# Kernel optimization log

Hardware: AMD Instinct MI355X
Metric: run time of the kernel (lower is better)

Reference implementation:

```python
import jax, jax.numpy as jnp
import numpy as np

N_NODES = 50000
N_EDGES = 800000
D_IN = 256
D_HID = 256
D_OUT = 8


def _glorot(key, shape):
    fan_in = shape[-1]
    bound = 1.0 / np.sqrt(fan_in)
    return jax.random.uniform(key, shape, minval=-bound, maxval=bound, dtype=jnp.float32)


def setup_inputs() -> dict:
    key = jax.random.key(0)
    ks = jax.random.split(key, 12)
    x = jax.random.normal(ks[0], (N_NODES, D_IN), dtype=jnp.float32)
    edge_index = jax.random.randint(ks[1], (2, N_EDGES), 0, N_NODES, dtype=jnp.int64)
    return {
        "x": x,
        "edge_index": edge_index,
        # SAGEConv1: lin_l (neighbor path, has bias), lin_r (root path, no bias)
        "W1l": _glorot(ks[2], (D_HID, D_IN)),
        "b1": jnp.zeros((D_HID,), jnp.float32),
        "W1r": _glorot(ks[3], (D_HID, D_IN)),
        # SAGEConv2
        "W2l": _glorot(ks[4], (D_HID, D_HID)),
        "b2": jnp.zeros((D_HID,), jnp.float32),
        "W2r": _glorot(ks[5], (D_HID, D_HID)),
        # MLP decoder
        "Wm1": _glorot(ks[6], (D_HID, D_HID)),
        "bm1": _glorot(ks[7], (D_HID,)),
        "Wm2": _glorot(ks[8], (D_OUT, D_HID)),
        "bm2": _glorot(ks[9], (D_OUT,)),
    }


def _sage_conv(x, edge_index, Wl, b, Wr):
    # PyG SAGEConv with mean aggregation:
    # out = lin_l(mean_{j in N(i)} x_j) + lin_r(x_i)
    src, dst = edge_index[0], edge_index[1]
    msg = x[src]  # [E, d] gather
    agg = jax.ops.segment_sum(msg, dst, num_segments=x.shape[0])  # [N, d]
    cnt = jax.ops.segment_sum(jnp.ones((edge_index.shape[1],), x.dtype), dst,
                              num_segments=x.shape[0])  # in-degree [N]
    mean = agg / jnp.maximum(cnt, 1.0)[:, None]
    return mean @ Wl.T + b + x @ Wr.T


def reference(x, edge_index, W1l, b1, W1r, W2l, b2, W2r, Wm1, bm1, Wm2, bm2):
    h = jax.nn.relu(_sage_conv(x, edge_index, W1l, b1, W1r))
    h = jax.nn.relu(_sage_conv(h, edge_index, W2l, b2, W2r))
    h = jax.nn.relu(h @ Wm1.T + bm1)
    logits = h @ Wm2.T + bm2
    return jax.nn.softmax(logits, axis=-1)
```

## Files before the change

kernel.cpp:

```cpp
#include <hip/hip_runtime.h>
#include <math.h>

#define N_NODES 50000
#define N_EDGES 800000
#define D 256

typedef unsigned short u16;
typedef __attribute__((ext_vector_type(8))) __bf16 bf16x8;
typedef __attribute__((ext_vector_type(4))) float f32x4;

__device__ __forceinline__ void split_hi_lo(float v, u16& h, u16& l) {
    unsigned u = __float_as_uint(v);
    unsigned hh = (u + 0x7fff + ((u >> 16) & 1)) >> 16;
    float hf = __uint_as_float(hh << 16);
    float res = v - hf;
    unsigned ul = __float_as_uint(res);
    unsigned ll = (ul + 0x7fff + ((ul >> 16) & 1)) >> 16;
    h = (u16)hh; l = (u16)ll;
}

__device__ __forceinline__ float bflo(unsigned u) { return __uint_as_float(u << 16); }
__device__ __forceinline__ float bfhi(unsigned u) { return __uint_as_float(u & 0xffff0000u); }

__device__ __forceinline__ void gl_lds16(const void* g, void* l) {
    __builtin_amdgcn_global_load_lds(
        (const __attribute__((address_space(1))) void*)g,
        (__attribute__((address_space(3))) void*)l, 16, 0, 0);
}

__global__ void zero_i32(int* __restrict__ p, int n) {
    int i = blockIdx.x * blockDim.x + threadIdx.x;
    if (i < n) p[i] = 0;
}

__global__ void count_deg(const int* __restrict__ ei, int* __restrict__ cnt) {
    int e = blockIdx.x * blockDim.x + threadIdx.x;
    if (e < N_EDGES) atomicAdd(&cnt[ei[N_EDGES + e]], 1);
}

__global__ void scan1(const int* __restrict__ cnt, int* __restrict__ partial,
                      int* __restrict__ bsum) {
    __shared__ int s[1024];
    int t = threadIdx.x, b = blockIdx.x;
    int gid = b * 1024 + t;
    int v = (gid < N_NODES) ? cnt[gid] : 0;
    s[t] = v;
    __syncthreads();
    for (int off = 1; off < 1024; off <<= 1) {
        int u = (t >= off) ? s[t - off] : 0;
        __syncthreads();
        s[t] += u;
        __syncthreads();
    }
    partial[gid] = s[t];
    if (t == 1023) bsum[b] = s[1023];
}

__global__ void scan2(const int* __restrict__ bsum, int* __restrict__ boff, int nb) {
    int t = threadIdx.x;
    int orig = (t < nb) ? bsum[t] : 0;
    int v = orig;
    #pragma unroll
    for (int off = 1; off < 64; off <<= 1) {
        int u = __shfl_up(v, off, 64);
        if (t >= off) v += u;
    }
    boff[t] = v - orig;
}

__global__ void scan3(const int* __restrict__ partial, const int* __restrict__ boff,
                      int* __restrict__ rowptr, int* __restrict__ cursor) {
    int i = blockIdx.x * blockDim.x + threadIdx.x;
    if (i <= N_NODES) {
        int val = 0;
        if (i > 0) val = partial[i - 1] + boff[(i - 1) >> 10];
        rowptr[i] = val;
        if (i < N_NODES) cursor[i] = val;
    }
}

__global__ void fill_edges(const int* __restrict__ ei, int* __restrict__ cursor,
                           int* __restrict__ esrc) {
    int e = blockIdx.x * blockDim.x + threadIdx.x;
    if (e < N_EDGES) {
        int p = atomicAdd(&cursor[ei[N_EDGES + e]], 1);
        esrc[p] = ei[e];
    }
}

__global__ void split_bf16(const float* __restrict__ in, u16* __restrict__ hi,
                           u16* __restrict__ lo, int n) {
    int i = blockIdx.x * blockDim.x + threadIdx.x;
    if (i < n) {
        u16 h, l; split_hi_lo(in[i], h, l);
        hi[i] = h; lo[i] = l;
    }
}

__global__ __launch_bounds__(256) void aggregate_bf16(const u16* __restrict__ in_hi,
        const int* __restrict__ rowptr, const int* __restrict__ esrc,
        u16* __restrict__ ohi, u16* __restrict__ olo) {
    int node = blockIdx.x * 4 + (threadIdx.x >> 6);
    if (node >= N_NODES) return;
    int lane = threadIdx.x & 63;
    int half = lane >> 5;
    int sub = lane & 31;
    int beg = rowptr[node], end = rowptr[node + 1];
    const u16* rowp = in_hi + sub * 8;

    float a0 = 0.f, a1 = 0.f, a2 = 0.f, a3 = 0.f;
    float a4 = 0.f, a5 = 0.f, a6 = 0.f, a7 = 0.f;

#define ACC8(v) \
    a0 += bflo(v.x); a1 += bfhi(v.x); a2 += bflo(v.y); a3 += bfhi(v.y); \
    a4 += bflo(v.z); a5 += bfhi(v.z); a6 += bflo(v.w); a7 += bfhi(v.w);

    int j = beg;
    for (; j + 8 <= end; j += 8) {
        int i0 = esrc[j + 0 + half];
        int i1 = esrc[j + 2 + half];
        int i2 = esrc[j + 4 + half];
        int i3 = esrc[j + 6 + half];
        uint4 r0 = *(const uint4*)(rowp + (size_t)i0 * D);
        uint4 r1 = *(const uint4*)(rowp + (size_t)i1 * D);
        uint4 r2 = *(const uint4*)(rowp + (size_t)i2 * D);
        uint4 r3 = *(const uint4*)(rowp + (size_t)i3 * D);
        ACC8(r0); ACC8(r1); ACC8(r2); ACC8(r3);
    }
    for (; j < end; j += 2) {
        int e = j + half;
        if (e < end) {
            uint4 r = *(const uint4*)(rowp + (size_t)esrc[e] * D);
            ACC8(r);
        }
    }
#undef ACC8

    a0 += __shfl_xor(a0, 32, 64); a1 += __shfl_xor(a1, 32, 64);
    a2 += __shfl_xor(a2, 32, 64); a3 += __shfl_xor(a3, 32, 64);
    a4 += __shfl_xor(a4, 32, 64); a5 += __shfl_xor(a5, 32, 64);
    a6 += __shfl_xor(a6, 32, 64); a7 += __shfl_xor(a7, 32, 64);

    if (lane < 32) {
        float inv = 1.f / (float)max(end - beg, 1);
        float m[8] = { a0 * inv, a1 * inv, a2 * inv, a3 * inv,
                       a4 * inv, a5 * inv, a6 * inv, a7 * inv };
        u16 h[8], l[8];
        #pragma unroll
        for (int k = 0; k < 8; ++k) split_hi_lo(m[k], h[k], l[k]);
        size_t o = (size_t)node * D + lane * 8;
        *(uint4*)(ohi + o) = make_uint4(h[0] | (h[1] << 16), h[2] | (h[3] << 16),
                                        h[4] | (h[5] << 16), h[6] | (h[7] << 16));
        *(uint4*)(olo + o) = make_uint4(l[0] | (l[1] << 16), l[2] | (l[3] << 16),
                                        l[4] | (l[5] << 16), l[6] | (l[7] << 16));
    }
}

__global__ __launch_bounds__(256, 2) void gemm_mfma(
        const u16* __restrict__ A1h, const u16* __restrict__ A1l,
        const u16* __restrict__ A2h, const u16* __restrict__ A2l,
        const u16* __restrict__ B1h, const u16* __restrict__ B1l,
        const u16* __restrict__ B2h, const u16* __restrict__ B2l,
        const float* __restrict__ bias, int K, int relu,
        float* __restrict__ Cf, u16* __restrict__ Chi, u16* __restrict__ Clo) {
    __shared__ u16 lds[4][128 * 32];
    const int t = threadIdx.x;
    const int lane = t & 63;
    const int w = t >> 6;
    const int wm = (w >> 1) * 64, wn = (w & 1) * 64;
    const int m0 = blockIdx.x * 128, n0 = blockIdx.y * 128;

    f32x4 acc[4][4] = {};

    const int tr = t >> 2;
    const int g = (t & 3) ^ ((t >> 3) & 3);
    const int lm = lane & 15;
    const int sw = (((lane >> 4) ^ ((lm >> 1) & 3))) * 8;

    for (int k0 = 0; k0 < K; k0 += 32) {
        const u16 *Ah, *Al, *Bh, *Bl; int ks;
        if (k0 < 256) { Ah = A1h; Al = A1l; Bh = B1h; Bl = B1l; ks = k0; }
        else          { Ah = A2h; Al = A2l; Bh = B2h; Bl = B2l; ks = k0 - 256; }

        __syncthreads();
        #pragma unroll
        for (int r = 0; r < 2; ++r) {
            int arow = m0 + r * 64 + tr; if (arow >= N_NODES) arow = N_NODES - 1;
            size_t aoff = (size_t)arow * D + ks + g * 8;
            size_t boff = (size_t)(n0 + r * 64 + tr) * D + ks + g * 8;
            int dst = r * 2048 + t * 8;
            gl_lds16(Ah + aoff, &lds[0][dst]);
            gl_lds16(Al + aoff, &lds[1][dst]);
            gl_lds16(Bh + boff, &lds[2][dst]);
            gl_lds16(Bl + boff, &lds[3][dst]);
        }
        __syncthreads();

        bf16x8 ah[4], al[4], bh[4], bl[4];
        #pragma unroll
        for (int i = 0; i < 4; ++i) {
            int offA = (wm + i * 16 + lm) * 32 + sw;
            ah[i] = *(const bf16x8*)&lds[0][offA];
            al[i] = *(const bf16x8*)&lds[1][offA];
            int offB = (wn + i * 16 + lm) * 32 + sw;
            bh[i] = *(const bf16x8*)&lds[2][offB];
            bl[i] = *(const bf16x8*)&lds[3][offB];
        }
        #pragma unroll
        for (int i = 0; i < 4; ++i) {
            #pragma unroll
            for (int j = 0; j < 4; ++j) {
                acc[i][j] = __builtin_amdgcn_mfma_f32_16x16x32_bf16(ah[i], bh[j], acc[i][j], 0, 0, 0);
                acc[i][j] = __builtin_amdgcn_mfma_f32_16x16x32_bf16(ah[i], bl[j], acc[i][j], 0, 0, 0);
                acc[i][j] = __builtin_amdgcn_mfma_f32_16x16x32_bf16(al[i], bh[j], acc[i][j], 0, 0, 0);
            }
        }
    }

    const int q = lane >> 4;
    #pragma unroll
    for (int j = 0; j < 4; ++j) {
        int col = n0 + wn + j * 16 + lm;
        float bb = bias[col];
        #pragma unroll
        for (int i = 0; i < 4; ++i) {
            int rowb = m0 + wm + i * 16 + q * 4;
            #pragma unroll
            for (int r = 0; r < 4; ++r) {
                int row = rowb + r;
                if (row < N_NODES) {
                    float v = acc[i][j][r] + bb;
                    if (relu) v = fmaxf(v, 0.f);
                    size_t o = (size_t)row * D + col;
                    if (Cf) Cf[o] = v;
                    if (Chi) {
                        u16 h, l; split_hi_lo(v, h, l);
                        Chi[o] = h; Clo[o] = l;
                    }
                }
            }
        }
    }
}

__global__ __launch_bounds__(256) void mlp2_softmax(const float* __restrict__ h,
        const float* __restrict__ W, const float* __restrict__ b,
        float* __restrict__ out) {
    int wid = threadIdx.x >> 6;
    int lane = threadIdx.x & 63;
    int n = blockIdx.x * 4 + wid;
    if (n >= N_NODES) return;

    float4 hv = ((const float4*)(h + (size_t)n * D))[lane];
    float acc[8];
    #pragma unroll
    for (int o = 0; o < 8; ++o) {
        float4 w = ((const float4*)(W + o * D))[lane];
        acc[o] = hv.x * w.x + hv.y * w.y + hv.z * w.z + hv.w * w.w;
    }
    #pragma unroll
    for (int o = 0; o < 8; ++o) {
        #pragma unroll
        for (int off = 32; off >= 1; off >>= 1)
            acc[o] += __shfl_xor(acc[o], off, 64);
    }
    if (lane == 0) {
        float v[8];
        float m = -1e30f;
        #pragma unroll
        for (int o = 0; o < 8; ++o) { v[o] = acc[o] + b[o]; m = fmaxf(m, v[o]); }
        float s = 0.f;
        #pragma unroll
        for (int o = 0; o < 8; ++o) { v[o] = expf(v[o] - m); s += v[o]; }
        float inv = 1.f / s;
        float4 o0 = make_float4(v[0] * inv, v[1] * inv, v[2] * inv, v[3] * inv);
        float4 o1 = make_float4(v[4] * inv, v[5] * inv, v[6] * inv, v[7] * inv);
        ((float4*)(out + (size_t)n * 8))[0] = o0;
        ((float4*)(out + (size_t)n * 8))[1] = o1;
    }
}

static inline size_t align_up(size_t x) { return (x + 255) & ~(size_t)255; }

extern "C" void kernel_launch(void* const* d_in, const int* in_sizes, int n_in,
                              void* d_out, int out_size, void* d_ws, size_t ws_size,
                              hipStream_t stream) {
    const float* x   = (const float*)d_in[0];
    const int*   ei  = (const int*)d_in[1];
    const float* W1l = (const float*)d_in[2];
    const float* b1  = (const float*)d_in[3];
    const float* W1r = (const float*)d_in[4];
    const float* W2l = (const float*)d_in[5];
    const float* b2  = (const float*)d_in[6];
    const float* W2r = (const float*)d_in[7];
    const float* Wm1 = (const float*)d_in[8];
    const float* bm1 = (const float*)d_in[9];
    const float* Wm2 = (const float*)d_in[10];
    const float* bm2 = (const float*)d_in[11];
    float* out = (float*)d_out;

    const size_t NF = (size_t)N_NODES * D;
    const size_t NW = (size_t)D * D;

    char* w = (char*)d_ws;
    u16* x_hi  = (u16*)w; w += align_up(NF * 2);
    u16* x_lo  = (u16*)w; w += align_up(NF * 2);
    u16* mn_hi = (u16*)w; w += align_up(NF * 2 * 2);
    u16* mn_lo = mn_hi + NF;
    u16* h1_hi = (u16*)w; w += align_up(NF * 2);
    u16* h1_lo = (u16*)w; w += align_up(NF * 2);
    u16* h2_hi = (u16*)w; w += align_up(NF * 2);
    u16* h2_lo = (u16*)w; w += align_up(NF * 2);
    u16* wbuf  = (u16*)w; w += align_up(NW * 2 * 10);
    u16* w1l_h = wbuf + 0 * NW; u16* w1l_l = wbuf + 1 * NW;
    u16* w1r_h = wbuf + 2 * NW; u16* w1r_l = wbuf + 3 * NW;
    u16* w2l_h = wbuf + 4 * NW; u16* w2l_l = wbuf + 5 * NW;
    u16* w2r_h = wbuf + 6 * NW; u16* w2r_l = wbuf + 7 * NW;
    u16* wm1_h = wbuf + 8 * NW; u16* wm1_l = wbuf + 9 * NW;
    int* cnt     = (int*)w; w += align_up((size_t)N_NODES * 4);
    int* rowptr  = (int*)w; w += align_up((size_t)(N_NODES + 1) * 4);
    int* cursor  = (int*)w; w += align_up((size_t)N_NODES * 4);
    int* partial = (int*)w; w += align_up((size_t)49 * 1024 * 4);
    int* bsum    = (int*)w; w += align_up((size_t)64 * 4);
    int* boff    = (int*)w; w += align_up((size_t)64 * 4);
    int* esrc    = (int*)w; w += align_up((size_t)N_EDGES * 4);
    float* h3 = (float*)mn_hi;

    zero_i32<<<(N_NODES + 255) / 256, 256, 0, stream>>>(cnt, N_NODES);
    count_deg<<<(N_EDGES + 255) / 256, 256, 0, stream>>>(ei, cnt);
    scan1<<<49, 1024, 0, stream>>>(cnt, partial, bsum);
    scan2<<<1, 64, 0, stream>>>(bsum, boff, 49);
    scan3<<<(N_NODES + 256) / 256, 256, 0, stream>>>(partial, boff, rowptr, cursor);
    fill_edges<<<(N_EDGES + 255) / 256, 256, 0, stream>>>(ei, cursor, esrc);

    split_bf16<<<(int)((NF + 255) / 256), 256, 0, stream>>>(x, x_hi, x_lo, (int)NF);
    split_bf16<<<(int)((NW + 255) / 256), 256, 0, stream>>>(W1l, w1l_h, w1l_l, (int)NW);
    split_bf16<<<(int)((NW + 255) / 256), 256, 0, stream>>>(W1r, w1r_h, w1r_l, (int)NW);
    split_bf16<<<(int)((NW + 255) / 256), 256, 0, stream>>>(W2l, w2l_h, w2l_l, (int)NW);
    split_bf16<<<(int)((NW + 255) / 256), 256, 0, stream>>>(W2r, w2r_h, w2r_l, (int)NW);
    split_bf16<<<(int)((NW + 255) / 256), 256, 0, stream>>>(Wm1, wm1_h, wm1_l, (int)NW);

    dim3 ggrid((N_NODES + 127) / 128, 2);
    int agrid = (N_NODES + 3) / 4;

    aggregate_bf16<<<agrid, 256, 0, stream>>>(x_hi, rowptr, esrc, mn_hi, mn_lo);
    gemm_mfma<<<ggrid, 256, 0, stream>>>(mn_hi, mn_lo, x_hi, x_lo,
                                         w1l_h, w1l_l, w1r_h, w1r_l,
                                         b1, 512, 1, nullptr, h1_hi, h1_lo);
    aggregate_bf16<<<agrid, 256, 0, stream>>>(h1_hi, rowptr, esrc, mn_hi, mn_lo);
    gemm_mfma<<<ggrid, 256, 0, stream>>>(mn_hi, mn_lo, h1_hi, h1_lo,
                                         w2l_h, w2l_l, w2r_h, w2r_l,
                                         b2, 512, 1, nullptr, h2_hi, h2_lo);
    gemm_mfma<<<ggrid, 256, 0, stream>>>(h2_hi, h2_lo, h2_hi, h2_lo,
                                         wm1_h, wm1_l, wm1_h, wm1_l,
                                         bm1, 256, 1, h3, nullptr, nullptr);
    mlp2_softmax<<<(N_NODES + 3) / 4, 256, 0, stream>>>(h3, Wm2, bm2, out);
}
```

Measured before the change: 562.6 us.

## Double-buffer LDS tiles in MFMA GEMM to overlap global loads with compute

The GEMM kernel now keeps two LDS tile buffers. It issues the global-to-LDS loads for the next K-slice before running the MFMAs on the current slice, and waits with vmcnt(0) plus a barrier only after the compute. This is meant to hide global-memory latency behind matrix math and to cut one barrier per iteration. In exchange, LDS use per block doubles, from 32KB to 64KB, which can limit occupancy.

Result: no change. 563.8 us (+0.2%).

```diff
diff --git a/kernel.cpp b/kernel.cpp
--- a/kernel.cpp
+++ b/kernel.cpp
@@ -156,6 +156,23 @@
     }
 }
 
+__device__ __forceinline__ void stage_tile(u16 (*ldsb)[128 * 32],
+        const u16* __restrict__ Ah, const u16* __restrict__ Al,
+        const u16* __restrict__ Bh, const u16* __restrict__ Bl,
+        int ks, int m0, int n0, int t, int tr, int g) {
+    #pragma unroll
+    for (int r = 0; r < 2; ++r) {
+        int arow = m0 + r * 64 + tr; if (arow >= N_NODES) arow = N_NODES - 1;
+        size_t aoff = (size_t)arow * D + ks + g * 8;
+        size_t boff = (size_t)(n0 + r * 64 + tr) * D + ks + g * 8;
+        int dst = r * 2048 + t * 8;
+        gl_lds16(Ah + aoff, &ldsb[0][dst]);
+        gl_lds16(Al + aoff, &ldsb[1][dst]);
+        gl_lds16(Bh + boff, &ldsb[2][dst]);
+        gl_lds16(Bl + boff, &ldsb[3][dst]);
+    }
+}
+
 __global__ __launch_bounds__(256, 2) void gemm_mfma(
         const u16* __restrict__ A1h, const u16* __restrict__ A1l,
         const u16* __restrict__ A2h, const u16* __restrict__ A2l,
@@ -163,7 +180,7 @@
         const u16* __restrict__ B2h, const u16* __restrict__ B2l,
         const float* __restrict__ bias, int K, int relu,
         float* __restrict__ Cf, u16* __restrict__ Chi, u16* __restrict__ Clo) {
-    __shared__ u16 lds[4][128 * 32];
+    __shared__ u16 lds[2][4][128 * 32];
     const int t = threadIdx.x;
     const int lane = t & 63;
     const int w = t >> 6;
@@ -177,34 +194,35 @@
     const int lm = lane & 15;
     const int sw = (((lane >> 4) ^ ((lm >> 1) & 3))) * 8;
 
+    {
+        const u16 *Ah, *Al, *Bh, *Bl;
+        Ah = A1h; Al = A1l; Bh = B1h; Bl = B1l;
+        stage_tile(lds[0], Ah, Al, Bh, Bl, 0, m0, n0, t, tr, g);
+    }
+    asm volatile("s_waitcnt vmcnt(0)" ::: "memory");
+    __builtin_amdgcn_s_barrier();
+
+    int cur = 0;
     for (int k0 = 0; k0 < K; k0 += 32) {
-        const u16 *Ah, *Al, *Bh, *Bl; int ks;
-        if (k0 < 256) { Ah = A1h; Al = A1l; Bh = B1h; Bl = B1l; ks = k0; }
-        else          { Ah = A2h; Al = A2l; Bh = B2h; Bl = B2l; ks = k0 - 256; }
-
-        __syncthreads();
-        #pragma unroll
-        for (int r = 0; r < 2; ++r) {
-            int arow = m0 + r * 64 + tr; if (arow >= N_NODES) arow = N_NODES - 1;
-            size_t aoff = (size_t)arow * D + ks + g * 8;
-            size_t boff = (size_t)(n0 + r * 64 + tr) * D + ks + g * 8;
-            int dst = r * 2048 + t * 8;
-            gl_lds16(Ah + aoff, &lds[0][dst]);
-            gl_lds16(Al + aoff, &lds[1][dst]);
-            gl_lds16(Bh + boff, &lds[2][dst]);
-            gl_lds16(Bl + boff, &lds[3][dst]);
-        }
-        __syncthreads();
+        const int nxt = cur ^ 1;
+        const bool has_next = (k0 + 32 < K);
+        if (has_next) {
+            int k1 = k0 + 32;
+            const u16 *Ah, *Al, *Bh, *Bl; int ks;
+            if (k1 < 256) { Ah = A1h; Al = A1l; Bh = B1h; Bl = B1l; ks = k1; }
+            else          { Ah = A2h; Al = A2l; Bh = B2h; Bl = B2l; ks = k1 - 256; }
+            stage_tile(lds[nxt], Ah, Al, Bh, Bl, ks, m0, n0, t, tr, g);
+        }
 
         bf16x8 ah[4], al[4], bh[4], bl[4];
         #pragma unroll
         for (int i = 0; i < 4; ++i) {
             int offA = (wm + i * 16 + lm) * 32 + sw;
-            ah[i] = *(const bf16x8*)&lds[0][offA];
-            al[i] = *(const bf16x8*)&lds[1][offA];
+            ah[i] = *(const bf16x8*)&lds[cur][0][offA];
+            al[i] = *(const bf16x8*)&lds[cur][1][offA];
             int offB = (wn + i * 16 + lm) * 32 + sw;
-            bh[i] = *(const bf16x8*)&lds[2][offB];
-            bl[i] = *(const bf16x8*)&lds[3][offB];
+            bh[i] = *(const bf16x8*)&lds[cur][2][offB];
+            bl[i] = *(const bf16x8*)&lds[cur][3][offB];
         }
         #pragma unroll
         for (int i = 0; i < 4; ++i) {
@@ -214,6 +232,12 @@
                 acc[i][j] = __builtin_amdgcn_mfma_f32_16x16x32_bf16(ah[i], bl[j], acc[i][j], 0, 0, 0);
                 acc[i][j] = __builtin_amdgcn_mfma_f32_16x16x32_bf16(al[i], bh[j], acc[i][j], 0, 0, 0);
             }
+        }
+
+        if (has_next) {
+            asm volatile("s_waitcnt vmcnt(0)" ::: "memory");
+            __builtin_amdgcn_s_barrier();
+            cur = nxt;
         }
     }
 
```

## Triple-buffer GEMM LDS loads with 256x128 tiles and unroll aggregation loop

Applied to the files above, without the earlier changes.

The GEMM moves from 128x128 tiles with two barriers per k-step to 256x128 tiles of 512 threads, using a 3-stage dynamic-LDS ring buffer. Loads are issued two steps ahead and waited on with explicit vmcnt, and the MFMA section runs under raised wave priority. Blocks use a grouped M/N mapping so tiles that share A rows run close together. The aggregation kernel adds a 16-edge unrolled loop to keep more gathers in flight. The cost is higher register and LDS pressure and only one block per CU.

After: 551.0 us. 2.1% less time.

```diff
diff --git a/kernel.cpp b/kernel.cpp
--- a/kernel.cpp
+++ b/kernel.cpp
@@ -8,6 +8,9 @@
 typedef unsigned short u16;
 typedef __attribute__((ext_vector_type(8))) __bf16 bf16x8;
 typedef __attribute__((ext_vector_type(4))) float f32x4;
+
+#define BUF_U16 24576
+#define NBUF 3
 
 __device__ __forceinline__ void split_hi_lo(float v, u16& h, u16& l) {
     unsigned u = __float_as_uint(v);
@@ -116,6 +119,26 @@
     a4 += bflo(v.z); a5 += bfhi(v.z); a6 += bflo(v.w); a7 += bfhi(v.w);
 
     int j = beg;
+    for (; j + 16 <= end; j += 16) {
+        int i0 = esrc[j +  0 + half];
+        int i1 = esrc[j +  2 + half];
+        int i2 = esrc[j +  4 + half];
+        int i3 = esrc[j +  6 + half];
+        int i4 = esrc[j +  8 + half];
+        int i5 = esrc[j + 10 + half];
+        int i6 = esrc[j + 12 + half];
+        int i7 = esrc[j + 14 + half];
+        uint4 r0 = *(const uint4*)(rowp + (size_t)i0 * D);
+        uint4 r1 = *(const uint4*)(rowp + (size_t)i1 * D);
+        uint4 r2 = *(const uint4*)(rowp + (size_t)i2 * D);
+        uint4 r3 = *(const uint4*)(rowp + (size_t)i3 * D);
+        uint4 r4 = *(const uint4*)(rowp + (size_t)i4 * D);
+        uint4 r5 = *(const uint4*)(rowp + (size_t)i5 * D);
+        uint4 r6 = *(const uint4*)(rowp + (size_t)i6 * D);
+        uint4 r7 = *(const uint4*)(rowp + (size_t)i7 * D);
+        ACC8(r0); ACC8(r1); ACC8(r2); ACC8(r3);
+        ACC8(r4); ACC8(r5); ACC8(r6); ACC8(r7);
+    }
     for (; j + 8 <= end; j += 8) {
         int i0 = esrc[j + 0 + half];
         int i1 = esrc[j + 2 + half];
@@ -156,56 +179,87 @@
     }
 }
 
-__global__ __launch_bounds__(256, 2) void gemm_mfma(
+__device__ __forceinline__ void stage256(u16* buf,
+        const u16* __restrict__ Ah, const u16* __restrict__ Al,
+        const u16* __restrict__ Bh, const u16* __restrict__ Bl,
+        int ks, int m0, int n0, int t) {
+    int tr = t >> 2;
+    int g  = (t & 3) ^ ((t >> 3) & 3);
+    size_t boff = (size_t)(n0 + tr) * D + ks + g * 8;
+    gl_lds16(Bh + boff, buf + 16384 + t * 8);
+    gl_lds16(Bl + boff, buf + 20480 + t * 8);
+    #pragma unroll
+    for (int r = 0; r < 2; ++r) {
+        int arow = m0 + r * 128 + tr; if (arow >= N_NODES) arow = N_NODES - 1;
+        size_t aoff = (size_t)arow * D + ks + g * 8;
+        gl_lds16(Ah + aoff, buf + r * 4096 + t * 8);
+        gl_lds16(Al + aoff, buf + 8192 + r * 4096 + t * 8);
+    }
+}
+
+__global__ __launch_bounds__(512, 1) void gemm_mfma(
         const u16* __restrict__ A1h, const u16* __restrict__ A1l,
         const u16* __restrict__ A2h, const u16* __restrict__ A2l,
         const u16* __restrict__ B1h, const u16* __restrict__ B1l,
         const u16* __restrict__ B2h, const u16* __restrict__ B2l,
         const float* __restrict__ bias, int K, int relu,
         float* __restrict__ Cf, u16* __restrict__ Chi, u16* __restrict__ Clo) {
-    __shared__ u16 lds[4][128 * 32];
+    extern __shared__ u16 sh[];
     const int t = threadIdx.x;
     const int lane = t & 63;
     const int w = t >> 6;
     const int wm = (w >> 1) * 64, wn = (w & 1) * 64;
-    const int m0 = blockIdx.x * 128, n0 = blockIdx.y * 128;
+
+    int bid = blockIdx.x;
+    int m_idx, n_idx;
+    if (bid < 384) {
+        m_idx = (bid >> 4) * 8 + (bid & 7);
+        n_idx = (bid >> 3) & 1;
+    } else {
+        int r = bid - 384;
+        m_idx = 192 + (r & 3);
+        n_idx = r >> 2;
+    }
+    const int m0 = m_idx * 256, n0 = n_idx * 128;
 
     f32x4 acc[4][4] = {};
 
-    const int tr = t >> 2;
-    const int g = (t & 3) ^ ((t >> 3) & 3);
     const int lm = lane & 15;
-    const int sw = (((lane >> 4) ^ ((lm >> 1) & 3))) * 8;
-
-    for (int k0 = 0; k0 < K; k0 += 32) {
-        const u16 *Ah, *Al, *Bh, *Bl; int ks;
-        if (k0 < 256) { Ah = A1h; Al = A1l; Bh = B1h; Bl = B1l; ks = k0; }
-        else          { Ah = A2h; Al = A2l; Bh = B2h; Bl = B2l; ks = k0 - 256; }
-
-        __syncthreads();
-        #pragma unroll
-        for (int r = 0; r < 2; ++r) {
-            int arow = m0 + r * 64 + tr; if (arow >= N_NODES) arow = N_NODES - 1;
-            size_t aoff = (size_t)arow * D + ks + g * 8;
-            size_t boff = (size_t)(n0 + r * 64 + tr) * D + ks + g * 8;
-            int dst = r * 2048 + t * 8;
-            gl_lds16(Ah + aoff, &lds[0][dst]);
-            gl_lds16(Al + aoff, &lds[1][dst]);
-            gl_lds16(Bh + boff, &lds[2][dst]);
-            gl_lds16(Bl + boff, &lds[3][dst]);
-        }
-        __syncthreads();
-
+    const int sw = ((lane >> 4) ^ ((lm >> 1) & 3)) * 8;
+    const int nsteps = K >> 5;
+
+    stage256(sh,           A1h, A1l, B1h, B1l,  0, m0, n0, t);
+    stage256(sh + BUF_U16, A1h, A1l, B1h, B1l, 32, m0, n0, t);
+
+    int cur = 0;
+    for (int s = 0; s < nsteps; ++s) {
+        if (s + 1 < nsteps) {
+            asm volatile("s_waitcnt vmcnt(6)" ::: "memory");
+        } else {
+            asm volatile("s_waitcnt vmcnt(0)" ::: "memory");
+        }
+        __builtin_amdgcn_s_barrier();
+        __builtin_amdgcn_sched_barrier(0);
+
+        if (s + 2 < nsteps) {
+            int sb = cur + 2; if (sb >= NBUF) sb -= NBUF;
+            int ksg = (s + 2) * 32;
+            if (ksg < 256) stage256(sh + sb * BUF_U16, A1h, A1l, B1h, B1l, ksg,       m0, n0, t);
+            else           stage256(sh + sb * BUF_U16, A2h, A2l, B2h, B2l, ksg - 256, m0, n0, t);
+        }
+
+        const u16* buf = sh + cur * BUF_U16;
         bf16x8 ah[4], al[4], bh[4], bl[4];
         #pragma unroll
         for (int i = 0; i < 4; ++i) {
             int offA = (wm + i * 16 + lm) * 32 + sw;
-            ah[i] = *(const bf16x8*)&lds[0][offA];
-            al[i] = *(const bf16x8*)&lds[1][offA];
+            ah[i] = *(const bf16x8*)(buf + offA);
+            al[i] = *(const bf16x8*)(buf + 8192 + offA);
             int offB = (wn + i * 16 + lm) * 32 + sw;
-            bh[i] = *(const bf16x8*)&lds[2][offB];
-            bl[i] = *(const bf16x8*)&lds[3][offB];
-        }
+            bh[i] = *(const bf16x8*)(buf + 16384 + offB);
+            bl[i] = *(const bf16x8*)(buf + 20480 + offB);
+        }
+        __builtin_amdgcn_s_setprio(1);
         #pragma unroll
         for (int i = 0; i < 4; ++i) {
             #pragma unroll
@@ -215,6 +269,9 @@
                 acc[i][j] = __builtin_amdgcn_mfma_f32_16x16x32_bf16(al[i], bh[j], acc[i][j], 0, 0, 0);
             }
         }
+        __builtin_amdgcn_s_setprio(0);
+
+        cur = (cur == NBUF - 1) ? 0 : cur + 1;
     }
 
     const int q = lane >> 4;
@@ -326,6 +383,14 @@
     int* esrc    = (int*)w; w += align_up((size_t)N_EDGES * 4);
     float* h3 = (float*)mn_hi;
 
+    static bool attr_done = false;
+    if (!attr_done) {
+        hipFuncSetAttribute((const void*)gemm_mfma,
+                            hipFuncAttributeMaxDynamicSharedMemorySize,
+                            NBUF * BUF_U16 * 2);
+        attr_done = true;
+    }
+
     zero_i32<<<(N_NODES + 255) / 256, 256, 0, stream>>>(cnt, N_NODES);
     count_deg<<<(N_EDGES + 255) / 256, 256, 0, stream>>>(ei, cnt);
     scan1<<<49, 1024, 0, stream>>>(cnt, partial, bsum);
@@ -340,19 +405,20 @@
     split_bf16<<<(int)((NW + 255) / 256), 256, 0, stream>>>(W2r, w2r_h, w2r_l, (int)NW);
     split_bf16<<<(int)((NW + 255) / 256), 256, 0, stream>>>(Wm1, wm1_h, wm1_l, (int)NW);
 
-    dim3 ggrid((N_NODES + 127) / 128, 2);
+    const int GEMM_LDS = NBUF * BUF_U16 * 2;
+    dim3 ggrid(392);
     int agrid = (N_NODES + 3) / 4;
 
     aggregate_bf16<<<agrid, 256, 0, stream>>>(x_hi, rowptr, esrc, mn_hi, mn_lo);
-    gemm_mfma<<<ggrid, 256, 0, stream>>>(mn_hi, mn_lo, x_hi, x_lo,
-                                         w1l_h, w1l_l, w1r_h, w1r_l,
-                                         b1, 512, 1, nullptr, h1_hi, h1_lo);
+    gemm_mfma<<<ggrid, 512, GEMM_LDS, stream>>>(mn_hi, mn_lo, x_hi, x_lo,
+                                                w1l_h, w1l_l, w1r_h, w1r_l,
+                                                b1, 512, 1, nullptr, h1_hi, h1_lo);
     aggregate_bf16<<<agrid, 256, 0, stream>>>(h1_hi, rowptr, esrc, mn_hi, mn_lo);
-    gemm_mfma<<<ggrid, 256, 0, stream>>>(mn_hi, mn_lo, h1_hi, h1_lo,
-                                         w2l_h, w2l_l, w2r_h, w2r_l,
-                                         b2, 512, 1, nullptr, h2_hi, h2_lo);
-    gemm_mfma<<<ggrid, 256, 0, stream>>>(h2_hi, h2_lo, h2_hi, h2_lo,
-                                         wm1_h, wm1_l, wm1_h, wm1_l,
-                                         bm1, 256, 1, h3, nullptr, nullptr);
+    gemm_mfma<<<ggrid, 512, GEMM_LDS, stream>>>(mn_hi, mn_lo, h1_hi, h1_lo,
+                                                w2l_h, w2l_l, w2r_h, w2r_l,
+                                                b2, 512, 1, nullptr, h2_hi, h2_lo);
+    gemm_mfma<<<ggrid, 512, GEMM_LDS, stream>>>(h2_hi, h2_lo, h2_hi, h2_lo,
+                                                wm1_h, wm1_l, wm1_h, wm1_l,
+                                                bm1, 256, 1, h3, nullptr, nullptr);
     mlp2_softmax<<<(N_NODES + 3) / 4, 256, 0, stream>>>(h3, Wm2, bm2, out);
 }
```
